# Kernel tuning notes

Measured on AMD Instinct MI355X. Metric: run time of the kernel, lower is better.

## Reference

```python
import jax, jax.numpy as jnp
import numpy as np

HEADS = 16
HEAD_DIM = 128
LAMBDA_INIT = 0.8
RMS_EPS = 1.1920928955078125e-07  # torch.finfo(float32).eps (RMSNorm eps=None default)


def setup_inputs() -> dict:
    key = jax.random.key(0)
    ks = jax.random.split(key, 9)
    b, s, d = 2, 2048, 2048
    x = jax.random.normal(ks[0], (b, s, d), dtype=jnp.float32)
    # torch Linear weights are (out_features, in_features); apply as x @ W.T
    wq = jax.random.normal(ks[1], (d, d), dtype=jnp.float32) * 0.02
    wk = jax.random.normal(ks[2], (d, d), dtype=jnp.float32) * 0.02
    wv = jax.random.normal(ks[3], (d, d), dtype=jnp.float32) * 0.02
    wo = jax.random.normal(ks[4], (d, d), dtype=jnp.float32) * 0.02
    # lambda vectors scaled small so exp(dot) stays finite
    lambda_q1 = jax.random.normal(ks[5], (HEAD_DIM,), dtype=jnp.float32) * 0.1
    lambda_q2 = jax.random.normal(ks[6], (HEAD_DIM,), dtype=jnp.float32) * 0.1
    lambda_k1 = jax.random.normal(ks[7], (HEAD_DIM,), dtype=jnp.float32) * 0.1
    lambda_k2 = jax.random.normal(ks[8], (HEAD_DIM,), dtype=jnp.float32) * 0.1
    return {"x": x, "wq": wq, "wk": wk, "wv": wv, "wo": wo,
            "lambda_q1": lambda_q1, "lambda_q2": lambda_q2,
            "lambda_k1": lambda_k1, "lambda_k2": lambda_k2}


def reference(x, wq, wk, wv, wo, lambda_q1, lambda_q2, lambda_k1, lambda_k2):
    b, s, d = x.shape
    h, hd = HEADS, HEAD_DIM
    # projections -> (b, h, s, hd)
    q = (x @ wq.T).reshape(b, s, h, hd).transpose(0, 2, 1, 3)
    k = (x @ wk.T).reshape(b, s, h, hd).transpose(0, 2, 1, 3)
    v = (x @ wv.T).reshape(b, s, h, hd).transpose(0, 2, 1, 3)
    q1, q2 = jnp.split(q, 2, axis=-1)
    k1, k2 = jnp.split(k, 2, axis=-1)
    # NOTE: source scales by sqrt(full head_dim), not the chunked dim
    scale = 1.0 / jnp.sqrt(jnp.float32(hd))
    a1 = jax.nn.softmax(jnp.einsum('bhqd,bhkd->bhqk', q1, k1) * scale, axis=-1)
    a2 = jax.nn.softmax(jnp.einsum('bhqd,bhkd->bhqk', q2, k2) * scale, axis=-1)
    lam = jnp.exp(jnp.dot(lambda_q1, lambda_k1)) - jnp.exp(jnp.dot(lambda_q2, lambda_k2)) + LAMBDA_INIT
    out = jnp.einsum('bhqk,bhkd->bhqd', a1 - lam * a2, v)  # (b,h,s,hd)
    # per-head RMSNorm (no affine) scaled by (1 - lambda_init)
    rms = jnp.sqrt(jnp.mean(out * out, axis=-1, keepdims=True) + RMS_EPS)
    normed = out / rms * (1.0 - LAMBDA_INIT)
    # faithful to torch: cat over heads on dim 1 -> (b, h*s, hd),
    # transpose(1,2) -> (b, hd, h*s), contiguous view -> (b, s, d)
    t = normed.reshape(b, h * s, hd).transpose(0, 2, 1).reshape(b, s, d)
    return t @ wo.T
```

## Files before the change

kernel.cpp:

```cpp
#include <hip/hip_runtime.h>
#include <hip/hip_bf16.h>
#include <cstdint>
#include <cstddef>

typedef __attribute__((ext_vector_type(8))) short short8;
typedef __attribute__((ext_vector_type(4))) float f4;
typedef __attribute__((ext_vector_type(4))) int i4;

#define MFMA16(a, b, c) __builtin_amdgcn_mfma_f32_16x16x32_bf16((a), (b), (c), 0, 0, 0)

__device__ __forceinline__ float bf2f(unsigned short u) {
    union { unsigned int i; float f; } v; v.i = ((unsigned int)u) << 16; return v.f;
}
__device__ __forceinline__ unsigned short f2bf(float f) {
    union { float f; unsigned int i; } v; v.f = f;
    unsigned int x = v.i;
    x += 0x7fffu + ((x >> 16) & 1u);
    return (unsigned short)(x >> 16);
}
__device__ __forceinline__ i4 pack8(const float* p) {
    f4 v0 = *(const f4*)p;
    f4 v1 = *(const f4*)(p + 4);
    unsigned int w0 = (unsigned int)f2bf(v0[0]) | ((unsigned int)f2bf(v0[1]) << 16);
    unsigned int w1 = (unsigned int)f2bf(v0[2]) | ((unsigned int)f2bf(v0[3]) << 16);
    unsigned int w2 = (unsigned int)f2bf(v1[0]) | ((unsigned int)f2bf(v1[1]) << 16);
    unsigned int w3 = (unsigned int)f2bf(v1[2]) | ((unsigned int)f2bf(v1[3]) << 16);
    i4 r; r[0] = (int)w0; r[1] = (int)w1; r[2] = (int)w2; r[3] = (int)w3; return r;
}
__device__ __forceinline__ void g2l16(const unsigned short* g, unsigned short* l) {
    __builtin_amdgcn_global_load_lds(
        (const __attribute__((address_space(1))) unsigned int*)g,
        (__attribute__((address_space(3))) unsigned int*)l,
        16, 0, 0);
}

static constexpr int S = 2048;
static constexpr int D = 2048;
static constexpr int H = 16;
static constexpr int HD = 128;
static constexpr int B = 2;

__global__ void detect_kernel(const unsigned short* __restrict__ w,
                              const void* __restrict__ lq1, const void* __restrict__ lq2,
                              const void* __restrict__ lk1, const void* __restrict__ lk2,
                              int* __restrict__ ctrl) {
    const int lane = threadIdx.x;
    int hits = 0;
    for (int j = 0; j < 4; j++) {
        unsigned short u = w[lane * 4 + j];
        hits += (((u >> 7) & 0xFF) >= 134) ? 1 : 0;
    }
    for (int m = 1; m <= 32; m <<= 1) hits += __shfl_xor(hits, m, 64);
    const int flag = (hits >= 16) ? 1 : 0;

    float d1 = 0.f, d2 = 0.f;
    for (int t = 0; t < 2; t++) {
        int e = lane + t * 64;
        float q1v, k1v, q2v, k2v;
        if (flag) {
            q1v = ((const float*)lq1)[e]; k1v = ((const float*)lk1)[e];
            q2v = ((const float*)lq2)[e]; k2v = ((const float*)lk2)[e];
        } else {
            q1v = bf2f(((const unsigned short*)lq1)[e]); k1v = bf2f(((const unsigned short*)lk1)[e]);
            q2v = bf2f(((const unsigned short*)lq2)[e]); k2v = bf2f(((const unsigned short*)lk2)[e]);
        }
        d1 += q1v * k1v; d2 += q2v * k2v;
    }
    for (int m = 1; m <= 32; m <<= 1) { d1 += __shfl_xor(d1, m, 64); d2 += __shfl_xor(d2, m, 64); }
    if (lane == 0) {
        ctrl[0] = flag;
        ctrl[1] = __float_as_int(__expf(d1) - __expf(d2) + 0.8f);
    }
}

__global__ __launch_bounds__(256) void conv_kernel(const void* __restrict__ src,
                                                   unsigned short* __restrict__ dst,
                                                   int n, const int* __restrict__ ctrl) {
    int i = (blockIdx.x * 256 + threadIdx.x) * 8;
    if (i >= n) return;
    if (ctrl[0]) *(i4*)&dst[i] = pack8(&((const float*)src)[i]);
    else         *(i4*)&dst[i] = *(const i4*)&((const unsigned short*)src)[i];
}

__global__ __launch_bounds__(256) void proj_kernel(
    const unsigned short* __restrict__ X,
    const unsigned short* __restrict__ Wq, const unsigned short* __restrict__ Wk,
    const unsigned short* __restrict__ Wv,
    unsigned short* __restrict__ Qb,
    unsigned short* __restrict__ Kb,
    unsigned short* __restrict__ Vt)
{
    const int zm = blockIdx.z;
    const unsigned short* __restrict__ W = (zm == 0) ? Wq : ((zm == 1) ? Wk : Wv);
    const int bm = blockIdx.x, bn = blockIdx.y;
    const int K = D;

    __shared__ __align__(16) unsigned short As[128 * 32];
    __shared__ __align__(16) unsigned short Bs[128 * 32];

    const int tid  = threadIdx.x;
    const int lane = tid & 63;
    const int wave = tid >> 6;
    const int quad = lane >> 4;
    const int l16  = lane & 15;
    const int wm   = (wave >> 1) * 64;
    const int wn   = (wave & 1) * 64;
    const int r0   = tid >> 2;
    const int koff = (tid & 3) * 8;

    f4 acc[4][4] = {};

    for (int k0 = 0; k0 < K; k0 += 32) {
        __syncthreads();
        g2l16(&X[(size_t)(bm * 128 + r0) * K + k0 + koff],
              (unsigned short*)((char*)As + wave * 1024));
        g2l16(&X[(size_t)(bm * 128 + r0 + 64) * K + k0 + koff],
              (unsigned short*)((char*)As + wave * 1024 + 4096));
        g2l16(&W[(size_t)(bn * 128 + r0) * K + k0 + koff],
              (unsigned short*)((char*)Bs + wave * 1024));
        g2l16(&W[(size_t)(bn * 128 + r0 + 64) * K + k0 + koff],
              (unsigned short*)((char*)Bs + wave * 1024 + 4096));
        __syncthreads();

        short8 a[4], b[4];
        #pragma unroll
        for (int i = 0; i < 4; i++) {
            a[i] = *(const short8*)&As[(wm + i * 16 + l16) * 32 + quad * 8];
            b[i] = *(const short8*)&Bs[(wn + i * 16 + l16) * 32 + quad * 8];
        }
        #pragma unroll
        for (int i = 0; i < 4; i++)
            #pragma unroll
            for (int j = 0; j < 4; j++)
                acc[i][j] = MFMA16(a[i], b[j], acc[i][j]);
    }

    for (int i = 0; i < 4; i++)
        for (int j = 0; j < 4; j++)
            for (int reg = 0; reg < 4; reg++) {
                int row = bm * 128 + wm + i * 16 + quad * 4 + reg;
                int col = bn * 128 + wn + j * 16 + l16;
                int b_idx = row >> 11, s0 = row & (S - 1);
                int h0 = col >> 7, e = col & (HD - 1);
                unsigned short val = f2bf(acc[i][j][reg]);
                if (zm == 2) {
                    Vt[(((size_t)(b_idx * H + h0)) * HD + e) * S + s0] = val;
                } else {
                    unsigned short* O = (zm == 0) ? Qb : Kb;
                    O[(((size_t)(b_idx * H + h0)) * S + s0) * HD + e] = val;
                }
            }
}

__global__ __launch_bounds__(256, 2) void attn_kernel(
    const unsigned short* __restrict__ Qb,
    const unsigned short* __restrict__ Kb,
    const unsigned short* __restrict__ Vt,
    const int* __restrict__ ctrl,
    unsigned short* __restrict__ Nm)
{
    const int h = blockIdx.y, b = blockIdx.z;
    const unsigned short* __restrict__ q  = Qb + ((size_t)(b * H + h)) * S * HD;
    const unsigned short* __restrict__ k  = Kb + ((size_t)(b * H + h)) * S * HD;
    const unsigned short* __restrict__ vt = Vt + ((size_t)(b * H + h)) * HD * S;
    const float lam = __int_as_float(ctrl[1]);

    const int tid  = threadIdx.x;
    const int lane = tid & 63;
    const int wave = tid >> 6;
    const int quad = lane >> 4;
    const int l16  = lane & 15;
    const int row0 = blockIdx.x * 64 + wave * 16;

    short8 aq1[2], aq2[2];
    #pragma unroll
    for (int t = 0; t < 2; t++) {
        aq1[t] = *(const short8*)&q[((size_t)(row0 + l16)) * HD + t * 32 + quad * 8];
        aq2[t] = *(const short8*)&q[((size_t)(row0 + l16)) * HD + 64 + t * 32 + quad * 8];
    }

    __shared__ __align__(16) unsigned short plds[4][2][16 * 32];

    float l1[4] = {}, l2[4] = {};
    f4 o1[8] = {}, o2[8] = {};
    const float scale = 0.08838834764831845f;

    unsigned short* pl1 = &plds[wave][0][0];
    unsigned short* pl2 = &plds[wave][1][0];

    #define LOADK(key0, kf)                                                              \
        {                                                                                \
            _Pragma("unroll") for (int v = 0; v < 2; v++)                                \
            _Pragma("unroll") for (int st = 0; st < 2; st++)                             \
            _Pragma("unroll") for (int t = 0; t < 2; t++)                                \
                kf[v][st][t] = *(const short8*)&k[(size_t)((key0) + 2 * l16 + st) * HD   \
                                                  + v * 64 + t * 32 + quad * 8];         \
        }
    #define LOADV(key0, vf)                                                              \
        {                                                                                \
            _Pragma("unroll") for (int f = 0; f < 8; f++)                                \
                vf[f] = *(const short8*)&vt[(size_t)(f * 16 + l16) * S + (key0) + quad * 8]; \
        }
    #define BODY(key0, kf, vf)                                                           \
        {                                                                                \
            f4 s1a = {}, s1b = {}, s2a = {}, s2b = {};                                   \
            _Pragma("unroll") for (int t = 0; t < 2; t++) {                              \
                s1a = MFMA16(aq1[t], kf[0][0][t], s1a);                                  \
                s1b = MFMA16(aq1[t], kf[0][1][t], s1b);                                  \
                s2a = MFMA16(aq2[t], kf[1][0][t], s2a);                                  \
                s2b = MFMA16(aq2[t], kf[1][1][t], s2b);                                  \
            }                                                                            \
            _Pragma("unroll") for (int r = 0; r < 4; r++) {                              \
                float pa1 = __expf(s1a[r] * scale);                                      \
                float pb1 = __expf(s1b[r] * scale);                                      \
                float pa2 = __expf(s2a[r] * scale);                                      \
                float pb2 = __expf(s2b[r] * scale);                                      \
                *(unsigned int*)&pl1[(quad * 4 + r) * 32 + 2 * l16] =                    \
                    (unsigned int)f2bf(pa1) | ((unsigned int)f2bf(pb1) << 16);           \
                *(unsigned int*)&pl2[(quad * 4 + r) * 32 + 2 * l16] =                    \
                    (unsigned int)f2bf(pa2) | ((unsigned int)f2bf(pb2) << 16);           \
                l1[r] += pa1 + pb1;                                                      \
                l2[r] += pa2 + pb2;                                                      \
            }                                                                            \
            short8 ap1 = *(const short8*)&pl1[l16 * 32 + quad * 8];                      \
            short8 ap2 = *(const short8*)&pl2[l16 * 32 + quad * 8];                      \
            _Pragma("unroll") for (int f = 0; f < 8; f++) {                              \
                o1[f] = MFMA16(ap1, vf[f], o1[f]);                                       \
                o2[f] = MFMA16(ap2, vf[f], o2[f]);                                       \
            }                                                                            \
        }

    short8 kA[2][2][2], kB[2][2][2], vA[8], vB[8];
    LOADK(0, kA); LOADV(0, vA);

    for (int key0 = 0; key0 < S; key0 += 64) {
        LOADK(key0 + 32, kB); LOADV(key0 + 32, vB);
        BODY(key0, kA, vA);
        int nx = (key0 + 64 < S) ? key0 + 64 : 0;
        LOADK(nx, kA); LOADV(nx, vA);
        BODY(key0 + 32, kB, vB);
    }
    #undef LOADK
    #undef LOADV
    #undef BODY

    #pragma unroll
    for (int r = 0; r < 4; r++)
        for (int mask = 1; mask <= 8; mask <<= 1) {
            l1[r] += __shfl_xor(l1[r], mask, 64);
            l2[r] += __shfl_xor(l2[r], mask, 64);
        }

    float ssq[4] = {};
    for (int f = 0; f < 8; f++)
        for (int r = 0; r < 4; r++) {
            float fin = o1[f][r] / l1[r] - lam * (o2[f][r] / l2[r]);
            o1[f][r] = fin;
            ssq[r] += fin * fin;
        }
    for (int r = 0; r < 4; r++)
        for (int mask = 1; mask <= 8; mask <<= 1)
            ssq[r] += __shfl_xor(ssq[r], mask, 64);

    for (int r = 0; r < 4; r++) {
        float rms = sqrtf(ssq[r] * (1.0f / 128.0f) + 1.1920928955078125e-07f);
        float sc = 0.2f / rms;
        int s0 = row0 + quad * 4 + r;
        for (int f = 0; f < 8; f++) {
            int e = f * 16 + l16;
            Nm[((size_t)b * D + (e * H + h)) * S + s0] = f2bf(o1[f][r] * sc);
        }
    }
}

__global__ __launch_bounds__(256) void out_kernel(
    const unsigned short* __restrict__ Nm,
    const unsigned short* __restrict__ Wo,
    const int* __restrict__ ctrl,
    void* __restrict__ Out)
{
    const int flag = ctrl[0];
    const int bz = blockIdx.z;
    const unsigned short* __restrict__ A = Nm + (size_t)bz * D * S;
    const int K = S;
    const int bm = blockIdx.x, bn = blockIdx.y;

    __shared__ __align__(16) unsigned short As[128 * 32];
    __shared__ __align__(16) unsigned short Bs[128 * 32];

    const int tid  = threadIdx.x;
    const int lane = tid & 63;
    const int wave = tid >> 6;
    const int quad = lane >> 4;
    const int l16  = lane & 15;
    const int wm   = (wave >> 1) * 64;
    const int wn   = (wave & 1) * 64;
    const int r0   = tid >> 2;
    const int koff = (tid & 3) * 8;

    f4 acc[4][4] = {};

    for (int k0 = 0; k0 < K; k0 += 32) {
        __syncthreads();
        g2l16(&A[(size_t)(bm * 128 + r0) * K + k0 + koff],
              (unsigned short*)((char*)As + wave * 1024));
        g2l16(&A[(size_t)(bm * 128 + r0 + 64) * K + k0 + koff],
              (unsigned short*)((char*)As + wave * 1024 + 4096));
        g2l16(&Wo[(size_t)(bn * 128 + r0) * K + k0 + koff],
              (unsigned short*)((char*)Bs + wave * 1024));
        g2l16(&Wo[(size_t)(bn * 128 + r0 + 64) * K + k0 + koff],
              (unsigned short*)((char*)Bs + wave * 1024 + 4096));
        __syncthreads();

        short8 a[4], b[4];
        #pragma unroll
        for (int i = 0; i < 4; i++) {
            a[i] = *(const short8*)&As[(wm + i * 16 + l16) * 32 + quad * 8];
            b[i] = *(const short8*)&Bs[(wn + i * 16 + l16) * 32 + quad * 8];
        }
        #pragma unroll
        for (int i = 0; i < 4; i++)
            #pragma unroll
            for (int j = 0; j < 4; j++)
                acc[i][j] = MFMA16(a[i], b[j], acc[i][j]);
    }

    for (int i = 0; i < 4; i++)
        for (int j = 0; j < 4; j++)
            for (int reg = 0; reg < 4; reg++) {
                int row = bm * 128 + wm + i * 16 + quad * 4 + reg;
                int col = bn * 128 + wn + j * 16 + l16;
                size_t idx = (size_t)bz * S * D + (size_t)row * D + col;
                if (flag) ((float*)Out)[idx] = acc[i][j][reg];
                else      ((unsigned short*)Out)[idx] = f2bf(acc[i][j][reg]);
            }
}

static constexpr size_t NEED_BYTES = 256 + 56ull * 1024 * 1024 * 2;
static void* g_extra = nullptr;

extern "C" void kernel_launch(void* const* d_in, const int* in_sizes, int n_in,
                              void* d_out, int out_size, void* d_ws, size_t ws_size,
                              hipStream_t stream) {
    const void* x   = d_in[0];
    const void* wq  = d_in[1];
    const void* wk  = d_in[2];
    const void* wv  = d_in[3];
    const void* wo  = d_in[4];
    const void* lq1 = d_in[5];
    const void* lq2 = d_in[6];
    const void* lk1 = d_in[7];
    const void* lk2 = d_in[8];

    char* base;
    if (ws_size >= NEED_BYTES) {
        base = (char*)d_ws;
    } else {
        if (!g_extra) (void)hipMalloc(&g_extra, NEED_BYTES);
        base = g_extra ? (char*)g_extra : (char*)d_ws;
    }

    int* ctrl = (int*)base;
    unsigned short* pw = (unsigned short*)(base + 256);
    const size_t NX = (size_t)B * S * D;
    const size_t NW = (size_t)D * D;
    const size_t NH = (size_t)B * H * S * HD;
    unsigned short* Xc  = pw;  pw += NX;
    unsigned short* Wqc = pw;  pw += NW;
    unsigned short* Wkc = pw;  pw += NW;
    unsigned short* Wvc = pw;  pw += NW;
    unsigned short* Woc = pw;  pw += NW;
    unsigned short* Qb  = pw;  pw += NH;
    unsigned short* Kb  = pw;  pw += NH;
    unsigned short* Vt  = pw;  pw += NH;
    unsigned short* Nm  = pw;

    detect_kernel<<<1, 64, 0, stream>>>((const unsigned short*)wq, lq1, lq2, lk1, lk2, ctrl);

    conv_kernel<<<(int)(NX / 2048), 256, 0, stream>>>(x,  Xc,  (int)NX, ctrl);
    conv_kernel<<<(int)(NW / 2048), 256, 0, stream>>>(wq, Wqc, (int)NW, ctrl);
    conv_kernel<<<(int)(NW / 2048), 256, 0, stream>>>(wk, Wkc, (int)NW, ctrl);
    conv_kernel<<<(int)(NW / 2048), 256, 0, stream>>>(wv, Wvc, (int)NW, ctrl);
    conv_kernel<<<(int)(NW / 2048), 256, 0, stream>>>(wo, Woc, (int)NW, ctrl);

    dim3 g1(32, 16, 3);
    proj_kernel<<<g1, 256, 0, stream>>>(Xc, Wqc, Wkc, Wvc, Qb, Kb, Vt);

    dim3 g2(S / 64, H, B);
    attn_kernel<<<g2, 256, 0, stream>>>(Qb, Kb, Vt, ctrl, Nm);

    dim3 g3(16, 16, 2);
    out_kernel<<<g3, 256, 0, stream>>>(Nm, Woc, ctrl, d_out);
}
```

Measured before the change: 803.5 us.

## Compute transposed scores to keep P in registers, dropping the LDS round-trip

Swaps the MFMA operand order so each lane holds the score tile transposed, which lets the probabilities feed the PV MFMA directly from registers instead of being written to and reread from shared memory. The V fragment loads are split into two 4-element halves to match the new key ordering. Row sums are now accumulated per lane and reduced once after the loop. exp is done with exp2 using a prescaled constant, bf16 packing uses v_cvt_pk_bf16_f32, and the final normalization multiplies by reciprocals instead of dividing. This removes LDS stores, loads and waits from the inner loop but doubles the number of V load instructions.

```diff
diff --git a/kernel.cpp b/kernel.cpp
--- a/kernel.cpp
+++ b/kernel.cpp
@@ -4,8 +4,12 @@
 #include <cstddef>
 
 typedef __attribute__((ext_vector_type(8))) short short8;
+typedef __attribute__((ext_vector_type(4))) short short4v;
 typedef __attribute__((ext_vector_type(4))) float f4;
 typedef __attribute__((ext_vector_type(4))) int i4;
+
+typedef union { short4v h[2]; short8 s; } v8_t;
+typedef union { unsigned int w[4]; short8 s; } pk8_t;
 
 #define MFMA16(a, b, c) __builtin_amdgcn_mfma_f32_16x16x32_bf16((a), (b), (c), 0, 0, 0)
 
@@ -179,85 +183,97 @@
         aq2[t] = *(const short8*)&q[((size_t)(row0 + l16)) * HD + 64 + t * 32 + quad * 8];
     }
 
-    __shared__ __align__(16) unsigned short plds[4][2][16 * 32];
-
-    float l1[4] = {}, l2[4] = {};
+    float l1 = 0.f, l2 = 0.f;
     f4 o1[8] = {}, o2[8] = {};
-    const float scale = 0.08838834764831845f;
-
-    unsigned short* pl1 = &plds[wave][0][0];
-    unsigned short* pl2 = &plds[wave][1][0];
+    const float scale2 = 0.08838834764831845f * 1.4426950408889634f;
 
     #define LOADK(key0, kf)                                                              \
         {                                                                                \
+            _Pragma("unroll") for (int tile = 0; tile < 2; tile++)                       \
             _Pragma("unroll") for (int v = 0; v < 2; v++)                                \
-            _Pragma("unroll") for (int st = 0; st < 2; st++)                             \
             _Pragma("unroll") for (int t = 0; t < 2; t++)                                \
-                kf[v][st][t] = *(const short8*)&k[(size_t)((key0) + 2 * l16 + st) * HD   \
-                                                  + v * 64 + t * 32 + quad * 8];         \
+                kf[tile][v][t] = *(const short8*)&k[(size_t)((key0) + tile * 16 + l16) * HD \
+                                                    + v * 64 + t * 32 + quad * 8];       \
         }
     #define LOADV(key0, vf)                                                              \
         {                                                                                \
-            _Pragma("unroll") for (int f = 0; f < 8; f++)                                \
-                vf[f] = *(const short8*)&vt[(size_t)(f * 16 + l16) * S + (key0) + quad * 8]; \
-        }
-    #define BODY(key0, kf, vf)                                                           \
+            _Pragma("unroll") for (int f = 0; f < 8; f++) {                              \
+                vf[f].h[0] = *(const short4v*)&vt[(size_t)(f * 16 + l16) * S             \
+                                                  + (key0) + quad * 4];                  \
+                vf[f].h[1] = *(const short4v*)&vt[(size_t)(f * 16 + l16) * S             \
+                                                  + (key0) + 16 + quad * 4];             \
+            }                                                                            \
+        }
+    #define BODY(kf, vf)                                                                 \
         {                                                                                \
-            f4 s1a = {}, s1b = {}, s2a = {}, s2b = {};                                   \
-            _Pragma("unroll") for (int t = 0; t < 2; t++) {                              \
-                s1a = MFMA16(aq1[t], kf[0][0][t], s1a);                                  \
-                s1b = MFMA16(aq1[t], kf[0][1][t], s1b);                                  \
-                s2a = MFMA16(aq2[t], kf[1][0][t], s2a);                                  \
-                s2b = MFMA16(aq2[t], kf[1][1][t], s2b);                                  \
+            f4 s1[2], s2[2];                                                             \
+            _Pragma("unroll") for (int tile = 0; tile < 2; tile++) {                     \
+                s1[tile] = (f4){};  s2[tile] = (f4){};                                   \
+                _Pragma("unroll") for (int t = 0; t < 2; t++) {                          \
+                    s1[tile] = MFMA16(kf[tile][0][t], aq1[t], s1[tile]);                 \
+                    s2[tile] = MFMA16(kf[tile][1][t], aq2[t], s2[tile]);                 \
+                }                                                                        \
             }                                                                            \
+            float p1[2][4], p2[2][4];                                                    \
+            _Pragma("unroll") for (int tile = 0; tile < 2; tile++)                       \
             _Pragma("unroll") for (int r = 0; r < 4; r++) {                              \
-                float pa1 = __expf(s1a[r] * scale);                                      \
-                float pb1 = __expf(s1b[r] * scale);                                      \
-                float pa2 = __expf(s2a[r] * scale);                                      \
-                float pb2 = __expf(s2b[r] * scale);                                      \
-                *(unsigned int*)&pl1[(quad * 4 + r) * 32 + 2 * l16] =                    \
-                    (unsigned int)f2bf(pa1) | ((unsigned int)f2bf(pb1) << 16);           \
-                *(unsigned int*)&pl2[(quad * 4 + r) * 32 + 2 * l16] =                    \
-                    (unsigned int)f2bf(pa2) | ((unsigned int)f2bf(pb2) << 16);           \
-                l1[r] += pa1 + pb1;                                                      \
-                l2[r] += pa2 + pb2;                                                      \
+                p1[tile][r] = __builtin_amdgcn_exp2f(s1[tile][r] * scale2);              \
+                p2[tile][r] = __builtin_amdgcn_exp2f(s2[tile][r] * scale2);              \
             }                                                                            \
-            short8 ap1 = *(const short8*)&pl1[l16 * 32 + quad * 8];                      \
-            short8 ap2 = *(const short8*)&pl2[l16 * 32 + quad * 8];                      \
+            l1 += ((p1[0][0] + p1[0][1]) + (p1[0][2] + p1[0][3]))                        \
+                + ((p1[1][0] + p1[1][1]) + (p1[1][2] + p1[1][3]));                       \
+            l2 += ((p2[0][0] + p2[0][1]) + (p2[0][2] + p2[0][3]))                        \
+                + ((p2[1][0] + p2[1][1]) + (p2[1][2] + p2[1][3]));                       \
+            pk8_t pa1, pa2;                                                              \
+            asm("v_cvt_pk_bf16_f32 %0, %1, %2" : "=v"(pa1.w[0]) : "v"(p1[0][0]), "v"(p1[0][1])); \
+            asm("v_cvt_pk_bf16_f32 %0, %1, %2" : "=v"(pa1.w[1]) : "v"(p1[0][2]), "v"(p1[0][3])); \
+            asm("v_cvt_pk_bf16_f32 %0, %1, %2" : "=v"(pa1.w[2]) : "v"(p1[1][0]), "v"(p1[1][1])); \
+            asm("v_cvt_pk_bf16_f32 %0, %1, %2" : "=v"(pa1.w[3]) : "v"(p1[1][2]), "v"(p1[1][3])); \
+            asm("v_cvt_pk_bf16_f32 %0, %1, %2" : "=v"(pa2.w[0]) : "v"(p2[0][0]), "v"(p2[0][1])); \
+            asm("v_cvt_pk_bf16_f32 %0, %1, %2" : "=v"(pa2.w[1]) : "v"(p2[0][2]), "v"(p2[0][3])); \
+            asm("v_cvt_pk_bf16_f32 %0, %1, %2" : "=v"(pa2.w[2]) : "v"(p2[1][0]), "v"(p2[1][1])); \
+            asm("v_cvt_pk_bf16_f32 %0, %1, %2" : "=v"(pa2.w[3]) : "v"(p2[1][2]), "v"(p2[1][3])); \
             _Pragma("unroll") for (int f = 0; f < 8; f++) {                              \
-                o1[f] = MFMA16(ap1, vf[f], o1[f]);                                       \
-                o2[f] = MFMA16(ap2, vf[f], o2[f]);                                       \
+                o1[f] = MFMA16(pa1.s, vf[f].s, o1[f]);                                   \
+                o2[f] = MFMA16(pa2.s, vf[f].s, o2[f]);                                   \
             }                                                                            \
         }
 
-    short8 kA[2][2][2], kB[2][2][2], vA[8], vB[8];
+    short8 kA[2][2][2], kB[2][2][2];
+    v8_t vA[8], vB[8];
     LOADK(0, kA); LOADV(0, vA);
 
     for (int key0 = 0; key0 < S; key0 += 64) {
         LOADK(key0 + 32, kB); LOADV(key0 + 32, vB);
-        BODY(key0, kA, vA);
+        BODY(kA, vA);
         int nx = (key0 + 64 < S) ? key0 + 64 : 0;
         LOADK(nx, kA); LOADV(nx, vA);
-        BODY(key0 + 32, kB, vB);
+        BODY(kB, vB);
     }
     #undef LOADK
     #undef LOADV
     #undef BODY
 
+    l1 += __shfl_xor(l1, 16, 64); l1 += __shfl_xor(l1, 32, 64);
+    l2 += __shfl_xor(l2, 16, 64); l2 += __shfl_xor(l2, 32, 64);
+
+    float il1[4], il2[4];
     #pragma unroll
-    for (int r = 0; r < 4; r++)
-        for (int mask = 1; mask <= 8; mask <<= 1) {
-            l1[r] += __shfl_xor(l1[r], mask, 64);
-            l2[r] += __shfl_xor(l2[r], mask, 64);
-        }
+    for (int r = 0; r < 4; r++) {
+        il1[r] = 1.0f / __shfl(l1, quad * 4 + r, 64);
+        il2[r] = lam  / __shfl(l2, quad * 4 + r, 64);
+    }
 
     float ssq[4] = {};
+    #pragma unroll
     for (int f = 0; f < 8; f++)
+        #pragma unroll
         for (int r = 0; r < 4; r++) {
-            float fin = o1[f][r] / l1[r] - lam * (o2[f][r] / l2[r]);
+            float fin = o1[f][r] * il1[r] - o2[f][r] * il2[r];
             o1[f][r] = fin;
             ssq[r] += fin * fin;
         }
+    #pragma unroll
     for (int r = 0; r < 4; r++)
         for (int mask = 1; mask <= 8; mask <<= 1)
             ssq[r] += __shfl_xor(ssq[r], mask, 64);
```

New measurement: 1.046 ms. 1.3x slower.
